# Kernel optimization log

Hardware: AMD Instinct MI355X
Metric: run time of the kernel (lower is better)

Reference implementation:

```python
import jax, jax.numpy as jnp
import numpy as np

B, H, S, D = 2, 16, 2048, 64

def setup_inputs() -> dict:
    key = jax.random.key(0)
    kq, kk, kv = jax.random.split(key, 3)
    q = jax.random.normal(kq, (B, H, S, D), dtype=jnp.float32)
    k = jax.random.normal(kk, (B, H, S, D), dtype=jnp.float32)
    v = jax.random.normal(kv, (B, H, S, D), dtype=jnp.float32)
    return {"q": q, "k": k, "v": v}

def reference(q, k, v):
    d_k = q.shape[-1]
    scale = 1.0 / jnp.sqrt(jnp.asarray(d_k, dtype=q.dtype))
    # scores: [B, H, Sq, Sk]
    scores = jnp.einsum("bhqd,bhkd->bhqk", q, k) * scale
    attn = jax.nn.softmax(scores, axis=-1)
    out = jnp.einsum("bhqk,bhkd->bhqd", attn, v)
    return out
```

## Files before the change

kernel.cpp:

```cpp
#include <hip/hip_runtime.h>
#include <math.h>

constexpr int Bc = 2, Hc = 16, Sc = 2048, Dc = 64;
constexpr int BQ = 128;
constexpr int BK = 64;
constexpr int NT = Sc / BK;

constexpr size_t WS_TILE  = 8192;
constexpr size_t WS_BH    = (size_t)NT * WS_TILE;
constexpr size_t WS_HALF  = (size_t)Bc * Hc * WS_BH;

typedef __attribute__((ext_vector_type(8))) short short8v;
typedef __attribute__((ext_vector_type(4))) float f32x4;
typedef __attribute__((ext_vector_type(4))) unsigned int uint4v;

__device__ __forceinline__ unsigned int cvt_pk_bf16(float lo, float hi) {
    unsigned int d;
    asm("v_cvt_pk_bf16_f32 %0, %1, %2" : "=v"(d) : "v"(lo), "v"(hi));
    return d;
}
__device__ __forceinline__ unsigned short to_bf16(float f) {
    unsigned int u = __float_as_uint(f);
    return (unsigned short)((u + 0x7FFFu + ((u >> 16) & 1u)) >> 16);
}
__device__ __forceinline__ void gload16(const void* g, void* l) {
    __builtin_amdgcn_global_load_lds(
        (const __attribute__((address_space(1))) void*)g,
        (__attribute__((address_space(3))) void*)l, 16, 0, 0);
}

__global__ __launch_bounds__(512, 2)
void prep_kernel(const float* __restrict__ K, const float* __restrict__ V,
                 unsigned char* __restrict__ ws)
{
    __shared__ unsigned short lv[4096];
    const int tid = threadIdx.x;
    const int b   = blockIdx.x;
    const int r   = tid >> 3;
    const int c8  = (tid & 7) * 8;

    if (b < 1024) {
        const int bh = b >> 5, t = b & 31;
        const float* src = V + (((size_t)bh * Sc + t * BK) + r) * Dc + c8;
        float4 f0 = *reinterpret_cast<const float4*>(src);
        float4 f1 = *reinterpret_cast<const float4*>(src + 4);
        float f[8] = {f0.x, f0.y, f0.z, f0.w, f1.x, f1.y, f1.z, f1.w};
#pragma unroll
        for (int m = 0; m < 8; ++m) {
            int d = c8 + m;
            lv[(d * 64 + r) ^ ((d & 7) << 3)] = to_bf16(f[m]);
        }
        __syncthreads();
        uint4v w = *reinterpret_cast<const uint4v*>(&lv[tid * 8]);
        *reinterpret_cast<uint4v*>(
            ws + WS_HALF + ((size_t)bh * NT + t) * WS_TILE + tid * 16) = w;
    } else {
        const int b2 = b - 1024;
        const int bh = b2 >> 5, t = b2 & 31;
        const float* src = K + (((size_t)bh * Sc + t * BK) + r) * Dc + c8;
        float4 f0 = *reinterpret_cast<const float4*>(src);
        float4 f1 = *reinterpret_cast<const float4*>(src + 4);
        uint4v w;
        w[0] = cvt_pk_bf16(f0.x, f0.y);
        w[1] = cvt_pk_bf16(f0.z, f0.w);
        w[2] = cvt_pk_bf16(f1.x, f1.y);
        w[3] = cvt_pk_bf16(f1.z, f1.w);
        int byte = (r * 128 + (tid & 7) * 16) ^ ((r & 7) << 4);
        *reinterpret_cast<uint4v*>(
            ws + ((size_t)bh * NT + t) * WS_TILE + byte) = w;
    }
}

__global__ __launch_bounds__(512, 2)
void attn_mfma_kernel(const float* __restrict__ Q,
                      const unsigned char* __restrict__ ws,
                      float* __restrict__ O)
{
    __shared__ __align__(16) unsigned int smem[16384];
    unsigned char* sB = reinterpret_cast<unsigned char*>(smem);

    const int tid  = threadIdx.x;
    const int wave = tid >> 6;
    const int lane = tid & 63;
    const int n    = lane & 15;
    const int qd   = lane >> 4;
    const int qw   = wave & 3;
    const int kh   = wave >> 2;

    const int hid = blockIdx.x;
    const int hk  = hid >> 3;
    const int bh  = (hid & 7) + 8 * (hk >> 4);
    const int q0  = (hk & 15) * BQ;

    const float* Qg = Q + ((size_t)bh * Sc + q0) * Dc;
    float*       Og = O + ((size_t)bh * Sc + q0) * Dc;
    const unsigned char* wsK = ws + (size_t)bh * WS_BH;
    const unsigned char* wsV = ws + WS_HALF + (size_t)bh * WS_BH;

    short8v q_frag[2][2];
#pragma unroll
    for (int qt = 0; qt < 2; ++qt)
#pragma unroll
        for (int kc = 0; kc < 2; ++kc) {
            const float* qrow = Qg + (qw * 32 + qt * 16 + n) * Dc + kc * 32 + qd * 8;
            float4 f0 = *reinterpret_cast<const float4*>(qrow);
            float4 f1 = *reinterpret_cast<const float4*>(qrow + 4);
            uint4v u;
            u[0] = cvt_pk_bf16(f0.x * 0.125f, f0.y * 0.125f);
            u[1] = cvt_pk_bf16(f0.z * 0.125f, f0.w * 0.125f);
            u[2] = cvt_pk_bf16(f1.x * 0.125f, f1.y * 0.125f);
            u[3] = cvt_pk_bf16(f1.z * 0.125f, f1.w * 0.125f);
            q_frag[qt][kc] = __builtin_bit_cast(short8v, u);
        }

    const f32x4 z = {0.f, 0.f, 0.f, 0.f};
    f32x4 o_acc[2][4] = {{z, z, z, z}, {z, z, z, z}};
    float l_part[2] = {0.f, 0.f};

    gload16(wsK + tid * 16,           sB + tid * 16);
    gload16(wsV + tid * 16,           sB + 32768 + tid * 16);
    gload16(wsK + WS_TILE + tid * 16, sB + 8192 + tid * 16);
    gload16(wsV + WS_TILE + tid * 16, sB + 32768 + 8192 + tid * 16);

    for (int kt = 0; kt < NT; ++kt) {
        {
            const int lt = (kt + 2 < NT) ? kt + 2 : NT - 1;
            size_t src = (size_t)lt * WS_TILE + tid * 16;
            int dst = ((kt + 2) & 3) * 8192 + tid * 16;
            gload16(wsK + src, sB + dst);
            gload16(wsV + src, sB + 32768 + dst);
        }

        asm volatile("s_waitcnt vmcnt(4)" ::: "memory");
        __builtin_amdgcn_s_barrier();

        const unsigned char* kb = sB + (kt & 3) * 8192;
        f32x4 st[2][2] = {{z, z}, {z, z}};
        __builtin_amdgcn_s_setprio(1);
#pragma unroll
        for (int nt = 0; nt < 2; ++nt)
#pragma unroll
            for (int kc = 0; kc < 2; ++kc) {
                int byte = ((kh * 32 + nt * 16 + n) * 128 + kc * 64 + qd * 16)
                           ^ ((n & 7) << 4);
                short8v kf = *reinterpret_cast<const short8v*>(kb + byte);
#pragma unroll
                for (int qt = 0; qt < 2; ++qt)
                    st[qt][nt] = __builtin_amdgcn_mfma_f32_16x16x32_bf16(
                        kf, q_frag[qt][kc], st[qt][nt], 0, 0, 0);
            }
        __builtin_amdgcn_s_setprio(0);

        short8v pf0, pf1;
#pragma unroll
        for (int qt = 0; qt < 2; ++qt) {
            float p00 = __expf(st[qt][0][0]), p01 = __expf(st[qt][0][1]);
            float p02 = __expf(st[qt][0][2]), p03 = __expf(st[qt][0][3]);
            float p10 = __expf(st[qt][1][0]), p11 = __expf(st[qt][1][1]);
            float p12 = __expf(st[qt][1][2]), p13 = __expf(st[qt][1][3]);
            l_part[qt] += ((p00 + p01) + (p02 + p03)) + ((p10 + p11) + (p12 + p13));

            unsigned int x0 = cvt_pk_bf16(p00, p01);
            unsigned int x1 = cvt_pk_bf16(p02, p03);
            unsigned int y0 = cvt_pk_bf16(p10, p11);
            unsigned int y1 = cvt_pk_bf16(p12, p13);
            asm("v_permlane32_swap_b32 %0, %1" : "+v"(x0), "+v"(y0));
            asm("v_permlane16_swap_b32 %0, %1" : "+v"(x0), "+v"(y0));
            asm("v_permlane32_swap_b32 %0, %1" : "+v"(x1), "+v"(y1));
            asm("v_permlane16_swap_b32 %0, %1" : "+v"(x1), "+v"(y1));
            uint4v pu; pu[0] = x0; pu[1] = x1; pu[2] = y0; pu[3] = y1;
            if (qt == 0) pf0 = __builtin_bit_cast(short8v, pu);
            else         pf1 = __builtin_bit_cast(short8v, pu);
        }

        const unsigned char* vb = sB + 32768 + (kt & 3) * 8192;
        __builtin_amdgcn_s_setprio(1);
#pragma unroll
        for (int dt = 0; dt < 4; ++dt) {
            int byte = ((dt * 16 + n) * 128 + kh * 64 + qd * 16) ^ ((n & 7) << 4);
            short8v vf = *reinterpret_cast<const short8v*>(vb + byte);
            o_acc[0][dt] = __builtin_amdgcn_mfma_f32_16x16x32_bf16(
                pf0, vf, o_acc[0][dt], 0, 0, 0);
            o_acc[1][dt] = __builtin_amdgcn_mfma_f32_16x16x32_bf16(
                pf1, vf, o_acc[1][dt], 0, 0, 0);
        }
        __builtin_amdgcn_s_setprio(0);
    }

    __syncthreads();

    float* mo = reinterpret_cast<float*>(smem);
    float* ml = reinterpret_cast<float*>(smem + 8192);
    if (kh == 1) {
#pragma unroll
        for (int qt = 0; qt < 2; ++qt) {
#pragma unroll
            for (int dt = 0; dt < 4; ++dt)
                *reinterpret_cast<f32x4*>(
                    &mo[(((qw * 64 + lane) * 2 + qt) * 4 + dt) * 4]) = o_acc[qt][dt];
            ml[(qw * 64 + lane) * 2 + qt] = l_part[qt];
        }
    }
    __syncthreads();
    if (kh == 0) {
#pragma unroll
        for (int qt = 0; qt < 2; ++qt) {
#pragma unroll
            for (int dt = 0; dt < 4; ++dt)
                o_acc[qt][dt] += *reinterpret_cast<const f32x4*>(
                    &mo[(((qw * 64 + lane) * 2 + qt) * 4 + dt) * 4]);
            l_part[qt] += ml[(qw * 64 + lane) * 2 + qt];
        }

#pragma unroll
        for (int qt = 0; qt < 2; ++qt) {
            float lp = l_part[qt];
            lp += __shfl_xor(lp, 16, 64);
            lp += __shfl_xor(lp, 32, 64);
#pragma unroll
            for (int r = 0; r < 4; ++r) {
                float lr  = __shfl(lp, qd * 4 + r, 64);
                float inv = 1.0f / lr;
#pragma unroll
                for (int dt = 0; dt < 4; ++dt) {
                    Og[(qw * 32 + qt * 16 + qd * 4 + r) * Dc + dt * 16 + n] =
                        o_acc[qt][dt][r] * inv;
                }
            }
        }
    }
}

extern "C" void kernel_launch(void* const* d_in, const int* in_sizes, int n_in,
                              void* d_out, int out_size, void* d_ws, size_t ws_size,
                              hipStream_t stream) {
    const float* q = (const float*)d_in[0];
    const float* k = (const float*)d_in[1];
    const float* v = (const float*)d_in[2];
    float*       o = (float*)d_out;
    unsigned char* ws = (unsigned char*)d_ws;

    prep_kernel<<<dim3(2048), 512, 0, stream>>>(k, v, ws);
    attn_mfma_kernel<<<dim3((Sc / BQ) * Bc * Hc), 512, 0, stream>>>(q, ws, o);
}
```

Baseline: 134.3 us.

## Load K/V MFMA fragments directly from global memory, bypassing LDS staging

Reworks the prep kernel to store K row-major and V transposed (d-major) in bf16, so each lane can read its MFMA fragments straight from global memory. The main loop drops the LDS ring buffer, the global_load_lds calls and the per-tile barriers. It replaces them with register double-buffered K fragments and per-phase V prefetch. This removes block-wide synchronisation and LDS traffic, but every wave now issues its own global/L2 loads, losing the sharing across waves and adding exposed memory latency.

```diff
diff --git a/kernel.cpp b/kernel.cpp
--- a/kernel.cpp
+++ b/kernel.cpp
@@ -3,12 +3,10 @@
 
 constexpr int Bc = 2, Hc = 16, Sc = 2048, Dc = 64;
 constexpr int BQ = 128;
-constexpr int BK = 64;
-constexpr int NT = Sc / BK;
-
-constexpr size_t WS_TILE  = 8192;
-constexpr size_t WS_BH    = (size_t)NT * WS_TILE;
-constexpr size_t WS_HALF  = (size_t)Bc * Hc * WS_BH;
+constexpr int NTW = 32;
+
+constexpr size_t WS_BH     = (size_t)Sc * Dc * 2;
+constexpr size_t WS_K_TOTAL = (size_t)Bc * Hc * WS_BH;
 
 typedef __attribute__((ext_vector_type(8))) short short8v;
 typedef __attribute__((ext_vector_type(4))) float f32x4;
@@ -22,11 +20,6 @@
 __device__ __forceinline__ unsigned short to_bf16(float f) {
     unsigned int u = __float_as_uint(f);
     return (unsigned short)((u + 0x7FFFu + ((u >> 16) & 1u)) >> 16);
-}
-__device__ __forceinline__ void gload16(const void* g, void* l) {
-    __builtin_amdgcn_global_load_lds(
-        (const __attribute__((address_space(1))) void*)g,
-        (__attribute__((address_space(3))) void*)l, 16, 0, 0);
 }
 
 __global__ __launch_bounds__(512, 2)
@@ -41,7 +34,7 @@
 
     if (b < 1024) {
         const int bh = b >> 5, t = b & 31;
-        const float* src = V + (((size_t)bh * Sc + t * BK) + r) * Dc + c8;
+        const float* src = V + (((size_t)bh * Sc + t * 64) + r) * Dc + c8;
         float4 f0 = *reinterpret_cast<const float4*>(src);
         float4 f1 = *reinterpret_cast<const float4*>(src + 4);
         float f[8] = {f0.x, f0.y, f0.z, f0.w, f1.x, f1.y, f1.z, f1.w};
@@ -51,13 +44,16 @@
             lv[(d * 64 + r) ^ ((d & 7) << 3)] = to_bf16(f[m]);
         }
         __syncthreads();
-        uint4v w = *reinterpret_cast<const uint4v*>(&lv[tid * 8]);
+        const int dd = tid >> 3, k0 = (tid & 7) * 8;
+        int base = (dd * 64 + k0) ^ ((dd & 7) << 3);
+        uint4v w = *reinterpret_cast<const uint4v*>(&lv[base]);
         *reinterpret_cast<uint4v*>(
-            ws + WS_HALF + ((size_t)bh * NT + t) * WS_TILE + tid * 16) = w;
+            ws + WS_K_TOTAL + (size_t)bh * WS_BH
+               + ((size_t)dd * Sc + t * 64 + k0) * 2) = w;
     } else {
         const int b2 = b - 1024;
         const int bh = b2 >> 5, t = b2 & 31;
-        const float* src = K + (((size_t)bh * Sc + t * BK) + r) * Dc + c8;
+        const float* src = K + (((size_t)bh * Sc + t * 64) + r) * Dc + c8;
         float4 f0 = *reinterpret_cast<const float4*>(src);
         float4 f1 = *reinterpret_cast<const float4*>(src + 4);
         uint4v w;
@@ -65,9 +61,8 @@
         w[1] = cvt_pk_bf16(f0.z, f0.w);
         w[2] = cvt_pk_bf16(f1.x, f1.y);
         w[3] = cvt_pk_bf16(f1.z, f1.w);
-        int byte = (r * 128 + (tid & 7) * 16) ^ ((r & 7) << 4);
         *reinterpret_cast<uint4v*>(
-            ws + ((size_t)bh * NT + t) * WS_TILE + byte) = w;
+            ws + (size_t)bh * WS_BH + (((size_t)t * 64 + r) * 64 + c8) * 2) = w;
     }
 }
 
@@ -76,8 +71,8 @@
                       const unsigned char* __restrict__ ws,
                       float* __restrict__ O)
 {
-    __shared__ __align__(16) unsigned int smem[16384];
-    unsigned char* sB = reinterpret_cast<unsigned char*>(smem);
+    __shared__ float mo[8192];
+    __shared__ float ml[512];
 
     const int tid  = threadIdx.x;
     const int wave = tid >> 6;
@@ -94,8 +89,11 @@
 
     const float* Qg = Q + ((size_t)bh * Sc + q0) * Dc;
     float*       Og = O + ((size_t)bh * Sc + q0) * Dc;
-    const unsigned char* wsK = ws + (size_t)bh * WS_BH;
-    const unsigned char* wsV = ws + WS_HALF + (size_t)bh * WS_BH;
+    const unsigned char* kP = ws + (size_t)bh * WS_BH;
+    const unsigned char* vP = ws + WS_K_TOTAL + (size_t)bh * WS_BH;
+
+    const size_t kOff = ((size_t)(kh * 1024 + n) * 64 + qd * 8) * 2;
+    const size_t vOff = ((size_t)n * Sc + kh * 1024 + qd * 8) * 2;
 
     short8v q_frag[2][2];
 #pragma unroll
@@ -117,80 +115,81 @@
     f32x4 o_acc[2][4] = {{z, z, z, z}, {z, z, z, z}};
     float l_part[2] = {0.f, 0.f};
 
-    gload16(wsK + tid * 16,           sB + tid * 16);
-    gload16(wsV + tid * 16,           sB + 32768 + tid * 16);
-    gload16(wsK + WS_TILE + tid * 16, sB + 8192 + tid * 16);
-    gload16(wsV + WS_TILE + tid * 16, sB + 32768 + 8192 + tid * 16);
-
-    for (int kt = 0; kt < NT; ++kt) {
-        {
-            const int lt = (kt + 2 < NT) ? kt + 2 : NT - 1;
-            size_t src = (size_t)lt * WS_TILE + tid * 16;
-            int dst = ((kt + 2) & 3) * 8192 + tid * 16;
-            gload16(wsK + src, sB + dst);
-            gload16(wsV + src, sB + 32768 + dst);
-        }
-
-        asm volatile("s_waitcnt vmcnt(4)" ::: "memory");
-        __builtin_amdgcn_s_barrier();
-
-        const unsigned char* kb = sB + (kt & 3) * 8192;
-        f32x4 st[2][2] = {{z, z}, {z, z}};
-        __builtin_amdgcn_s_setprio(1);
-#pragma unroll
-        for (int nt = 0; nt < 2; ++nt)
-#pragma unroll
-            for (int kc = 0; kc < 2; ++kc) {
-                int byte = ((kh * 32 + nt * 16 + n) * 128 + kc * 64 + qd * 16)
-                           ^ ((n & 7) << 4);
-                short8v kf = *reinterpret_cast<const short8v*>(kb + byte);
-#pragma unroll
-                for (int qt = 0; qt < 2; ++qt)
-                    st[qt][nt] = __builtin_amdgcn_mfma_f32_16x16x32_bf16(
-                        kf, q_frag[qt][kc], st[qt][nt], 0, 0, 0);
-            }
-        __builtin_amdgcn_s_setprio(0);
-
-        short8v pf0, pf1;
-#pragma unroll
-        for (int qt = 0; qt < 2; ++qt) {
-            float p00 = __expf(st[qt][0][0]), p01 = __expf(st[qt][0][1]);
-            float p02 = __expf(st[qt][0][2]), p03 = __expf(st[qt][0][3]);
-            float p10 = __expf(st[qt][1][0]), p11 = __expf(st[qt][1][1]);
-            float p12 = __expf(st[qt][1][2]), p13 = __expf(st[qt][1][3]);
-            l_part[qt] += ((p00 + p01) + (p02 + p03)) + ((p10 + p11) + (p12 + p13));
-
-            unsigned int x0 = cvt_pk_bf16(p00, p01);
-            unsigned int x1 = cvt_pk_bf16(p02, p03);
-            unsigned int y0 = cvt_pk_bf16(p10, p11);
-            unsigned int y1 = cvt_pk_bf16(p12, p13);
-            asm("v_permlane32_swap_b32 %0, %1" : "+v"(x0), "+v"(y0));
-            asm("v_permlane16_swap_b32 %0, %1" : "+v"(x0), "+v"(y0));
-            asm("v_permlane32_swap_b32 %0, %1" : "+v"(x1), "+v"(y1));
-            asm("v_permlane16_swap_b32 %0, %1" : "+v"(x1), "+v"(y1));
-            uint4v pu; pu[0] = x0; pu[1] = x1; pu[2] = y0; pu[3] = y1;
-            if (qt == 0) pf0 = __builtin_bit_cast(short8v, pu);
-            else         pf1 = __builtin_bit_cast(short8v, pu);
-        }
-
-        const unsigned char* vb = sB + 32768 + (kt & 3) * 8192;
-        __builtin_amdgcn_s_setprio(1);
-#pragma unroll
-        for (int dt = 0; dt < 4; ++dt) {
-            int byte = ((dt * 16 + n) * 128 + kh * 64 + qd * 16) ^ ((n & 7) << 4);
-            short8v vf = *reinterpret_cast<const short8v*>(vb + byte);
-            o_acc[0][dt] = __builtin_amdgcn_mfma_f32_16x16x32_bf16(
-                pf0, vf, o_acc[0][dt], 0, 0, 0);
-            o_acc[1][dt] = __builtin_amdgcn_mfma_f32_16x16x32_bf16(
-                pf1, vf, o_acc[1][dt], 0, 0, 0);
-        }
-        __builtin_amdgcn_s_setprio(0);
-    }
-
-    __syncthreads();
-
-    float* mo = reinterpret_cast<float*>(smem);
-    float* ml = reinterpret_cast<float*>(smem + 8192);
+#define LKF(d0, d1, d2, d3, t)                                                  \
+    d0 = *reinterpret_cast<const short8v*>(kP + kOff + (size_t)(t) * 4096);     \
+    d1 = *reinterpret_cast<const short8v*>(kP + kOff + (size_t)(t) * 4096 + 64);\
+    d2 = *reinterpret_cast<const short8v*>(kP + kOff + (size_t)(t) * 4096 + 2048);\
+    d3 = *reinterpret_cast<const short8v*>(kP + kOff + (size_t)(t) * 4096 + 2112)
+#define LVF(t)                                                                  \
+    vf0 = *reinterpret_cast<const short8v*>(vP + vOff + (size_t)(t) * 64);      \
+    vf1 = *reinterpret_cast<const short8v*>(vP + vOff + (size_t)(t) * 64 + 65536);\
+    vf2 = *reinterpret_cast<const short8v*>(vP + vOff + (size_t)(t) * 64 + 131072);\
+    vf3 = *reinterpret_cast<const short8v*>(vP + vOff + (size_t)(t) * 64 + 196608)
+
+    short8v ka0, ka1, ka2, ka3, kb0, kb1, kb2, kb3;
+    short8v vf0, vf1, vf2, vf3;
+    LKF(ka0, ka1, ka2, ka3, 0);
+    LVF(0);
+
+#define SOFTMAX_ROUTE(stq, pfout)                                               \
+    {                                                                           \
+        float p00 = __expf(stq[0][0]), p01 = __expf(stq[0][1]);                 \
+        float p02 = __expf(stq[0][2]), p03 = __expf(stq[0][3]);                 \
+        float p10 = __expf(stq[1][0]), p11 = __expf(stq[1][1]);                 \
+        float p12 = __expf(stq[1][2]), p13 = __expf(stq[1][3]);                 \
+        lsum += ((p00 + p01) + (p02 + p03)) + ((p10 + p11) + (p12 + p13));      \
+        unsigned int x0 = cvt_pk_bf16(p00, p01);                                \
+        unsigned int x1 = cvt_pk_bf16(p02, p03);                                \
+        unsigned int y0 = cvt_pk_bf16(p10, p11);                                \
+        unsigned int y1 = cvt_pk_bf16(p12, p13);                                \
+        asm("v_permlane32_swap_b32 %0, %1" : "+v"(x0), "+v"(y0));               \
+        asm("v_permlane16_swap_b32 %0, %1" : "+v"(x0), "+v"(y0));               \
+        asm("v_permlane32_swap_b32 %0, %1" : "+v"(x1), "+v"(y1));               \
+        asm("v_permlane16_swap_b32 %0, %1" : "+v"(x1), "+v"(y1));               \
+        uint4v pu; pu[0] = x0; pu[1] = x1; pu[2] = y0; pu[3] = y1;              \
+        pfout = __builtin_bit_cast(short8v, pu);                                \
+    }
+
+#define PHASE(K0, K1, K2, K3, KN0, KN1, KN2, KN3, tkf, tvf)                     \
+    {                                                                           \
+        f32x4 st[2][2] = {{z, z}, {z, z}};                                      \
+        __builtin_amdgcn_s_setprio(1);                                          \
+        st[0][0] = __builtin_amdgcn_mfma_f32_16x16x32_bf16(K0, q_frag[0][0], st[0][0], 0, 0, 0); \
+        st[1][0] = __builtin_amdgcn_mfma_f32_16x16x32_bf16(K0, q_frag[1][0], st[1][0], 0, 0, 0); \
+        st[0][0] = __builtin_amdgcn_mfma_f32_16x16x32_bf16(K1, q_frag[0][1], st[0][0], 0, 0, 0); \
+        st[1][0] = __builtin_amdgcn_mfma_f32_16x16x32_bf16(K1, q_frag[1][1], st[1][0], 0, 0, 0); \
+        st[0][1] = __builtin_amdgcn_mfma_f32_16x16x32_bf16(K2, q_frag[0][0], st[0][1], 0, 0, 0); \
+        st[1][1] = __builtin_amdgcn_mfma_f32_16x16x32_bf16(K2, q_frag[1][0], st[1][1], 0, 0, 0); \
+        st[0][1] = __builtin_amdgcn_mfma_f32_16x16x32_bf16(K3, q_frag[0][1], st[0][1], 0, 0, 0); \
+        st[1][1] = __builtin_amdgcn_mfma_f32_16x16x32_bf16(K3, q_frag[1][1], st[1][1], 0, 0, 0); \
+        __builtin_amdgcn_s_setprio(0);                                          \
+        LKF(KN0, KN1, KN2, KN3, tkf);                 \
+        short8v pf0, pf1;                                                       \
+        { float& lsum = l_part[0]; SOFTMAX_ROUTE(st[0], pf0); }                 \
+        { float& lsum = l_part[1]; SOFTMAX_ROUTE(st[1], pf1); }                 \
+        __builtin_amdgcn_s_setprio(1);                                          \
+        o_acc[0][0] = __builtin_amdgcn_mfma_f32_16x16x32_bf16(pf0, vf0, o_acc[0][0], 0, 0, 0); \
+        o_acc[1][0] = __builtin_amdgcn_mfma_f32_16x16x32_bf16(pf1, vf0, o_acc[1][0], 0, 0, 0); \
+        o_acc[0][1] = __builtin_amdgcn_mfma_f32_16x16x32_bf16(pf0, vf1, o_acc[0][1], 0, 0, 0); \
+        o_acc[1][1] = __builtin_amdgcn_mfma_f32_16x16x32_bf16(pf1, vf1, o_acc[1][1], 0, 0, 0); \
+        o_acc[0][2] = __builtin_amdgcn_mfma_f32_16x16x32_bf16(pf0, vf2, o_acc[0][2], 0, 0, 0); \
+        o_acc[1][2] = __builtin_amdgcn_mfma_f32_16x16x32_bf16(pf1, vf2, o_acc[1][2], 0, 0, 0); \
+        o_acc[0][3] = __builtin_amdgcn_mfma_f32_16x16x32_bf16(pf0, vf3, o_acc[0][3], 0, 0, 0); \
+        o_acc[1][3] = __builtin_amdgcn_mfma_f32_16x16x32_bf16(pf1, vf3, o_acc[1][3], 0, 0, 0); \
+        __builtin_amdgcn_s_setprio(0);                                          \
+        LVF(tvf);                         \
+    }
+
+    for (int t = 0; t < NTW; t += 2) {
+        const int tA = (t + 2 < NTW) ? t + 2 : NTW - 1;
+        PHASE(ka0, ka1, ka2, ka3, kb0, kb1, kb2, kb3, t + 1, t + 1);
+        PHASE(kb0, kb1, kb2, kb3, ka0, ka1, ka2, ka3, tA, tA);
+    }
+#undef PHASE
+#undef SOFTMAX_ROUTE
+#undef LKF
+#undef LVF
+
     if (kh == 1) {
 #pragma unroll
         for (int qt = 0; qt < 2; ++qt) {
```

Measured after the change: 210.6 us. +56.8%, slower.
